# Kernel optimization log

Measured on AMD Instinct MI355X. Metric: run time of the kernel, lower is better.

Reference implementation:

```python
import jax, jax.numpy as jnp
import numpy as np

# static config (matches init_kwargs)
B = 16
S = 32          # patch grid side
td = 2          # tile_dim
ts = td * td    # tile size
T = (S // td) ** 2
R = 1           # register tokens
U = 1           # tile_comp_size
P = S * S
N = R + P
KC = T * U
K = R + KC
D = 768
H = 12
DH = D // H
HID = 32        # CPB hidden


def setup_inputs() -> dict:
    key = jax.random.key(0)
    ks = jax.random.split(key, 11)
    sc = 0.02
    x = jax.random.normal(ks[0], (B, N, D), jnp.float32)
    logit_w = jax.random.normal(ks[1], (U, D), jnp.float32) * sc
    q_w = jax.random.normal(ks[2], (D, D), jnp.float32) * sc
    kv_w = jax.random.normal(ks[3], (2 * D, D), jnp.float32) * sc
    out_w = jax.random.normal(ks[4], (D, D), jnp.float32) * sc
    out_b = jax.random.normal(ks[5], (D,), jnp.float32) * sc
    cpb_w1 = jax.random.normal(ks[6], (HID, 3), jnp.float32) * 0.5
    cpb_b1 = jax.random.normal(ks[7], (HID,), jnp.float32) * sc
    cpb_w2 = jax.random.normal(ks[8], (H, HID), jnp.float32) * 0.1
    cpb_b2 = jax.random.normal(ks[9], (H,), jnp.float32) * sc
    u_pos = jax.random.normal(ks[10], (1, U, 3), jnp.float32) * sc
    # query patch positions [qx, qy, 0] on the SxS grid (row-major)
    coords = np.arange(S, dtype=np.float32)
    gy, gx = np.meshgrid(coords, coords, indexing='ij')
    P_pos = np.stack([gx.ravel(), gy.ravel(), np.zeros(P, np.float32)], axis=-1)[:, None, :]
    # per-tile centers [cx, cy, 0], tile index t = row_tile*(S//td)+col_tile
    tc = np.arange(S // td, dtype=np.float32) * td + (td - 1) / 2.0
    ty, tx = np.meshgrid(tc, tc, indexing='ij')
    tile_centers = np.stack([tx.ravel(), ty.ravel(), np.zeros(T, np.float32)], axis=-1)[:, None, :]
    return {
        'x': x, 'logit_w': logit_w, 'q_w': q_w, 'kv_w': kv_w,
        'out_w': out_w, 'out_b': out_b,
        'cpb_w1': cpb_w1, 'cpb_b1': cpb_b1, 'cpb_w2': cpb_w2, 'cpb_b2': cpb_b2,
        'u_pos': u_pos,
        'P_pos': jnp.asarray(P_pos), 'tile_centers': jnp.asarray(tile_centers),
    }


def _cpb_bias(P_pos, tile_centers, u_pos, cpb_w1, cpb_b1, cpb_w2, cpb_b2, dtype):
    # anchors: tile center + tied per-U offset -> [KC, 3]
    k_pos = (tile_centers + u_pos).reshape(KC, 3)
    delta = P_pos - k_pos[None, :, :].reshape(1, KC, 3)  # [P, KC, 3]
    dxy, s_feat = delta[..., :2], delta[..., 2:]
    phi_xy = jnp.sign(dxy) * jnp.log1p(jnp.abs(dxy))
    feats = jnp.concatenate([phi_xy, -s_feat], axis=-1)  # [P, KC, 3]
    h = jax.nn.gelu(feats @ cpb_w1.T + cpb_b1, approximate=False)
    out_ctx = h @ cpb_w2.T + cpb_b2  # [P, KC, H]
    bias = jnp.zeros((N, K, H), dtype).at[R:, R:, :].set(out_ctx.astype(dtype))
    return bias.transpose(2, 0, 1)  # [H, N, K]


def reference(x, logit_w, q_w, kv_w, out_w, out_b,
              cpb_w1, cpb_b1, cpb_w2, cpb_b2, u_pos, P_pos, tile_centers):
    Bx = x.shape[0]
    # --- tiled softmax-weighted compression ---
    patch = x[:, R:, :].reshape(Bx, S // td, td, S // td, td, D)
    tiled = patch.transpose(0, 1, 3, 2, 4, 5).reshape(Bx, T, ts, D)  # [B,T,ts,D]
    scores = jnp.einsum('btsd,ud->btsu', tiled, logit_w)             # [B,T,ts,U]
    w = jax.nn.softmax(scores.astype(jnp.float32).transpose(0, 1, 3, 2), axis=-1)
    w = w.astype(scores.dtype)                                       # [B,T,U,ts]
    ctx_learn = jnp.einsum('btus,btsd->btud', w, tiled).reshape(Bx, T * U, D)
    ctx = jnp.concatenate([x[:, :R, :], ctx_learn], axis=1)          # [B,K,D]
    # --- projections ---
    q = jnp.einsum('bnd,ed->bne', x, q_w).reshape(Bx, N, H, DH).transpose(0, 2, 1, 3)
    kv = jnp.einsum('bkd,ed->bke', ctx, kv_w).reshape(Bx, K, 2, H, DH)
    k = kv[:, :, 0].transpose(0, 2, 1, 3)  # [B,H,K,DH]
    v = kv[:, :, 1].transpose(0, 2, 1, 3)
    # --- CPB additive bias + SDPA ---
    bias = _cpb_bias(P_pos, tile_centers, u_pos, cpb_w1, cpb_b1, cpb_w2, cpb_b2, x.dtype)
    scale = DH ** -0.5
    logits = jnp.einsum('bhnd,bhkd->bhnk', q, k) * scale + bias[None]
    attn = jax.nn.softmax(logits, axis=-1)
    o = jnp.einsum('bhnk,bhkd->bhnd', attn, v).transpose(0, 2, 1, 3).reshape(Bx, N, D)
    return o @ out_w.T + out_b
```

## Files before the change

### kernel.cpp

```cpp
#include <hip/hip_runtime.h>
#include <math.h>

namespace {
constexpr int BB   = 16;
constexpr int SS   = 32;
constexpr int TT   = 256;
constexpr int PP   = 1024;
constexpr int NTOK = 1025;
constexpr int KCC  = 256;
constexpr int KTOK = 257;
constexpr int DD   = 768;
constexpr int HH   = 12;
constexpr int DHH  = 64;
constexpr int BNP  = 1040;
}

typedef _Float16 f16x8 __attribute__((ext_vector_type(8)));
typedef _Float16 f16x2 __attribute__((ext_vector_type(2)));
typedef float f32x4 __attribute__((ext_vector_type(4)));

#define GLOAD_LDS16(gsrc, ldst)                                               \
  __builtin_amdgcn_global_load_lds(                                           \
      (const __attribute__((address_space(1))) unsigned int*)(gsrc),          \
      (__attribute__((address_space(3))) unsigned int*)(ldst), 16, 0, 0)

__global__ __launch_bounds__(256) void cvt_weights_kernel(
    const float* __restrict__ q_w, const float* __restrict__ kv_w,
    const float* __restrict__ out_w,
    _Float16* __restrict__ qwh, _Float16* __restrict__ kvwh,
    _Float16* __restrict__ owh) {
  constexpr int NQ = DD * DD;
  constexpr int NK = 2 * DD * DD;
  const int i = (blockIdx.x * 256 + threadIdx.x) * 8;
  const float* src;
  _Float16* dst;
  int off;
  float scale = 1.0f;
  if (i < NQ) { src = q_w; dst = qwh; off = i; scale = 0.125f; }
  else if (i < NQ + NK) { src = kv_w; dst = kvwh; off = i - NQ; }
  else if (i < NQ + NK + NQ) { src = out_w; dst = owh; off = i - NQ - NK; }
  else return;
  const float4 a = *(const float4*)(src + off);
  const float4 b = *(const float4*)(src + off + 4);
  f16x8 o;
  o[0] = (_Float16)(a.x * scale); o[1] = (_Float16)(a.y * scale);
  o[2] = (_Float16)(a.z * scale); o[3] = (_Float16)(a.w * scale);
  o[4] = (_Float16)(b.x * scale); o[5] = (_Float16)(b.y * scale);
  o[6] = (_Float16)(b.z * scale); o[7] = (_Float16)(b.w * scale);
  *(f16x8*)(dst + off) = o;
}

__global__ __launch_bounds__(256) void ctx_kernel(
    const float* __restrict__ x, const float* __restrict__ logit_w,
    _Float16* __restrict__ ctxh, _Float16* __restrict__ xh) {
  const int blk = blockIdx.x;
  const int b = blk >> 8;
  const int t = blk & 255;
  const int tid = threadIdx.x;
  const int lane = tid & 63;
  const int w = tid >> 6;
  const float* xb = x + (size_t)b * NTOK * DD;
  _Float16* xhb = xh + (size_t)b * NTOK * DD;

  int prow[4];
#pragma unroll
  for (int s = 0; s < 4; ++s)
    prow[s] = 1 + ((t >> 4) * 2 + (s >> 1)) * SS + ((t & 15) * 2 + (s & 1));

  float sv[3][4];
  float part[4] = {0.f, 0.f, 0.f, 0.f};
#pragma unroll
  for (int it = 0; it < 3; ++it) {
    const int d = tid + 256 * it;
    const float lw = logit_w[d];
#pragma unroll
    for (int s = 0; s < 4; ++s) {
      const float xv = xb[(size_t)prow[s] * DD + d];
      sv[it][s] = xv;
      part[s] += xv * lw;
      xhb[(size_t)prow[s] * DD + d] = (_Float16)xv;
    }
  }

#pragma unroll
  for (int dd = 1; dd < 64; dd <<= 1)
#pragma unroll
    for (int s = 0; s < 4; ++s) part[s] += __shfl_xor(part[s], dd, 64);
  __shared__ float wred[4][4];
  if (lane == 0)
#pragma unroll
    for (int s = 0; s < 4; ++s) wred[w][s] = part[s];
  __syncthreads();
  float score[4];
#pragma unroll
  for (int s = 0; s < 4; ++s)
    score[s] = wred[0][s] + wred[1][s] + wred[2][s] + wred[3][s];

  const float mx = fmaxf(fmaxf(score[0], score[1]), fmaxf(score[2], score[3]));
  float e[4], sum = 0.f;
#pragma unroll
  for (int s = 0; s < 4; ++s) { e[s] = expf(score[s] - mx); sum += e[s]; }
  const float inv = 1.f / sum;
#pragma unroll
  for (int s = 0; s < 4; ++s) e[s] *= inv;

  _Float16* crow = ctxh + ((size_t)b * KTOK + 1 + t) * DD;
#pragma unroll
  for (int it = 0; it < 3; ++it) {
    const int d = tid + 256 * it;
    float acc = 0.f;
#pragma unroll
    for (int s = 0; s < 4; ++s) acc += e[s] * sv[it][s];
    crow[d] = (_Float16)acc;
  }
  if (t == 0) {
    _Float16* dst = ctxh + (size_t)b * KTOK * DD;
#pragma unroll
    for (int it = 0; it < 3; ++it) {
      const int d = tid + 256 * it;
      const float xv = xb[d];
      dst[d] = (_Float16)xv;
      xhb[d] = (_Float16)xv;
    }
  }
}

template <int OUTF16>
__global__ __launch_bounds__(256) void gemm_f16_kernel(
    const _Float16* __restrict__ A, const _Float16* __restrict__ W,
    const float* __restrict__ bias, void* __restrict__ Cout,
    int M, int Nout, int gx) {
  constexpr int BK = 64;
  __shared__ _Float16 As[128 * BK];
  __shared__ _Float16 Ws[128 * BK];

  const int tid = threadIdx.x;
  const int lane = tid & 63;
  const int w = tid >> 6;
  const int fr = lane & 15;
  const int g = lane >> 4;
  const int awm = (w >> 1) * 64;
  const int awn = (w & 1) * 64;

  const int nwg = gridDim.x;
  const int q8 = nwg >> 3, r8 = nwg & 7;
  const int xcd = blockIdx.x & 7;
  const int base = (xcd < r8) ? xcd * (q8 + 1) : r8 * (q8 + 1) + (xcd - r8) * q8;
  const int wg = base + (blockIdx.x >> 3);
  const int row0 = (wg / gx) * 128;
  const int col0 = (wg % gx) * 128;

  const int srow = lane >> 3;
  const int schunk = (lane & 7) ^ (srow & 7);

  f32x4 acc[4][4];
#pragma unroll
  for (int i = 0; i < 4; ++i)
#pragma unroll
    for (int j = 0; j < 4; ++j) acc[i][j] = (f32x4){0.f, 0.f, 0.f, 0.f};

  for (int k0 = 0; k0 < 768; k0 += BK) {
    __syncthreads();
#pragma unroll
    for (int c = 0; c < 4; ++c) {
      const int rl = w * 32 + c * 8 + srow;
      int ga = row0 + rl;
      ga = ga < M ? ga : M - 1;
      GLOAD_LDS16(A + (size_t)ga * 768 + k0 + schunk * 8, &As[(w * 32 + c * 8) * BK]);
      GLOAD_LDS16(W + (size_t)(col0 + rl) * 768 + k0 + schunk * 8,
                  &Ws[(w * 32 + c * 8) * BK]);
    }
    __syncthreads();

#pragma unroll
    for (int ks = 0; ks < 2; ++ks) {
      f16x8 af[4], bf[4];
#pragma unroll
      for (int i = 0; i < 4; ++i) {
        const int row = awm + i * 16 + fr;
        af[i] = *(const f16x8*)&As[row * BK + (((ks * 4 + g) ^ (fr & 7)) * 8)];
      }
#pragma unroll
      for (int j = 0; j < 4; ++j) {
        const int row = awn + j * 16 + fr;
        bf[j] = *(const f16x8*)&Ws[row * BK + (((ks * 4 + g) ^ (fr & 7)) * 8)];
      }
#pragma unroll
      for (int i = 0; i < 4; ++i)
#pragma unroll
        for (int j = 0; j < 4; ++j)
          acc[i][j] = __builtin_amdgcn_mfma_f32_16x16x32_f16(af[i], bf[j], acc[i][j], 0, 0, 0);
    }
  }

#pragma unroll
  for (int i = 0; i < 4; ++i) {
    const int rbase = row0 + awm + i * 16 + g * 4;
#pragma unroll
    for (int reg = 0; reg < 4; ++reg) {
      const int gr = rbase + reg;
      if (gr >= M) continue;
      if constexpr (OUTF16) {
        _Float16* crow = (_Float16*)Cout + (size_t)gr * Nout + col0;
#pragma unroll
        for (int j = 0; j < 4; ++j)
          crow[awn + j * 16 + fr] = (_Float16)acc[i][j][reg];
      } else {
        float* crow = (float*)Cout + (size_t)gr * Nout + col0;
#pragma unroll
        for (int j = 0; j < 4; ++j) {
          const int gc = awn + j * 16 + fr;
          crow[gc] = acc[i][j][reg] + bias[col0 + gc];
        }
      }
    }
  }
}

__global__ __launch_bounds__(256) void cpb_kernel(
    const float* __restrict__ P_pos, const float* __restrict__ tile_centers,
    const float* __restrict__ u_pos,
    const float* __restrict__ w1, const float* __restrict__ b1,
    const float* __restrict__ w2, const float* __restrict__ b2,
    float* __restrict__ biasK) {
  const int idx = blockIdx.x * 256 + threadIdx.x;
  const int c = idx >> 10;
  const int p = idx & 1023;

  const float px = P_pos[p * 3 + 0], py = P_pos[p * 3 + 1], pz = P_pos[p * 3 + 2];
  const float kx = tile_centers[c * 3 + 0] + u_pos[0];
  const float ky = tile_centers[c * 3 + 1] + u_pos[1];
  const float kz = tile_centers[c * 3 + 2] + u_pos[2];
  const float dx = px - kx, dy = py - ky, dz = pz - kz;
  const float fx = copysignf(log1pf(fabsf(dx)), dx);
  const float fy = copysignf(log1pf(fabsf(dy)), dy);
  const float fz = -dz;

  float outh[HH];
#pragma unroll
  for (int h = 0; h < HH; ++h) outh[h] = b2[h];
  for (int j = 0; j < 32; ++j) {
    float hj = fx * w1[j * 3 + 0] + fy * w1[j * 3 + 1] + fz * w1[j * 3 + 2] + b1[j];
    hj = 0.5f * hj * (1.f + erff(hj * 0.70710678118654752f));
#pragma unroll
    for (int h = 0; h < HH; ++h) outh[h] += hj * w2[h * 32 + j];
  }
#pragma unroll
  for (int h = 0; h < HH; ++h) {
    float* row = biasK + ((size_t)h * KCC + c) * BNP;
    row[1 + p] = outh[h];
    if (p == 0) row[0] = 0.f;
    if (p < BNP - 1 - PP) row[1 + PP + p] = 0.f;
  }
}

__global__ __launch_bounds__(512) void attn_mfma_kernel(
    const _Float16* __restrict__ qf, const _Float16* __restrict__ kvf,
    const float* __restrict__ biasK, _Float16* __restrict__ of) {
  __shared__ _Float16 Kh[4][64 * 64];
  __shared__ _Float16 Kt[16 * 64];
  __shared__ _Float16 Vt[4][64 * 64];
  __shared__ _Float16 Vtt[64 * 64];
  __shared__ _Float16 Pl[8][16 * 64];

  const int tid = threadIdx.x;
  const int lane = tid & 63;
  const int w = tid >> 6;
  const int fr = lane & 15;
  const int g = lane >> 4;

  const int b = blockIdx.x / HH;
  const int h = blockIdx.x % HH;

  if (tid < 256) {
    const int ksr = tid >> 2;
    const int kc0 = (tid & 3) * 2;
    const int s7 = ksr & 7;
#pragma unroll
    for (int kt = 0; kt < 4; ++kt) {
      const int key = kt * 64 + ksr;
      const _Float16* srcK = kvf + ((size_t)b * KTOK + key) * (2 * DD) + h * DHH;
      *(f16x8*)&Kh[kt][ksr * 64 + ((kc0 ^ s7) * 8)] = *(const f16x8*)(srcK + kc0 * 8);
      *(f16x8*)&Kh[kt][ksr * 64 + (((kc0 + 1) ^ s7) * 8)] = *(const f16x8*)(srcK + kc0 * 8 + 8);
    }
    if (ksr < 16) {
      const int key = min(256 + ksr, KTOK - 1);
      const _Float16* srcK = kvf + ((size_t)b * KTOK + key) * (2 * DD) + h * DHH;
      *(f16x8*)&Kt[ksr * 64 + ((kc0 ^ s7) * 8)] = *(const f16x8*)(srcK + kc0 * 8);
      *(f16x8*)&Kt[ksr * 64 + (((kc0 + 1) ^ s7) * 8)] = *(const f16x8*)(srcK + kc0 * 8 + 8);
    }
  } else {
    const int t2 = tid - 256;
    const int vkp = t2 & 31;
    const int vdh = (t2 >> 5) * 8;
#pragma unroll
    for (int kt = 0; kt < 4; ++kt) {
      const int kv0 = kt * 64 + 2 * vkp;
      const f16x8 va = *(const f16x8*)(kvf + ((size_t)b * KTOK + kv0) * (2 * DD) + DD + h * DHH + vdh);
      const f16x8 vbv = *(const f16x8*)(kvf + ((size_t)b * KTOK + kv0 + 1) * (2 * DD) + DD + h * DHH + vdh);
#pragma unroll
      for (int e = 0; e < 8; ++e) {
        const int d = vdh + e;
        f16x2 pr; pr[0] = va[e]; pr[1] = vbv[e];
        *(f16x2*)&Vt[kt][d * 64 + (((vkp >> 2) ^ (d & 7)) * 8) + 2 * (vkp & 3)] = pr;
      }
    }
    if (vkp < 16) {
      const int kv0 = min(256 + 2 * vkp, KTOK - 1);
      const int kv1 = min(256 + 2 * vkp + 1, KTOK - 1);
      const f16x8 va = *(const f16x8*)(kvf + ((size_t)b * KTOK + kv0) * (2 * DD) + DD + h * DHH + vdh);
      const f16x8 vbv = *(const f16x8*)(kvf + ((size_t)b * KTOK + kv1) * (2 * DD) + DD + h * DHH + vdh);
#pragma unroll
      for (int e = 0; e < 8; ++e) {
        const int d = vdh + e;
        f16x2 pr; pr[0] = va[e]; pr[1] = vbv[e];
        *(f16x2*)&Vtt[d * 64 + (((vkp >> 2) ^ (d & 7)) * 8) + 2 * (vkp & 3)] = pr;
      }
    }
  }
  __syncthreads();

  for (int c = w; c < 65; c += 8) {
    const int qc = c * 16;

    const int qrow = min(qc + fr, NTOK - 1);
    const _Float16* qsrc = qf + ((size_t)b * NTOK + qrow) * DD + h * DHH;
    f16x8 qa[2];
#pragma unroll
    for (int ks = 0; ks < 2; ++ks)
      qa[ks] = *(const f16x8*)(qsrc + ks * 32 + g * 8);

    float mr_[4], lr_[4];
#pragma unroll
    for (int r = 0; r < 4; ++r) { mr_[r] = -3.0e38f; lr_[r] = 0.f; }
    f32x4 outacc[4];
#pragma unroll
    for (int j = 0; j < 4; ++j) outacc[j] = (f32x4){0.f, 0.f, 0.f, 0.f};

    const int nb = min(qc + g * 4, PP);

#pragma unroll
    for (int kt = 0; kt < 4; ++kt) {
      const int k0 = kt * 64;
      f32x4 sf[4];
      __builtin_amdgcn_s_setprio(1);
#pragma unroll
      for (int f = 0; f < 4; ++f) {
        sf[f] = (f32x4){0.f, 0.f, 0.f, 0.f};
#pragma unroll
        for (int ks = 0; ks < 2; ++ks) {
          const f16x8 kf = *(const f16x8*)&Kh[kt][(f * 16 + fr) * 64 + (((ks * 4 + g) ^ (fr & 7)) * 8)];
          sf[f] = __builtin_amdgcn_mfma_f32_16x16x32_f16(qa[ks], kf, sf[f], 0, 0, 0);
        }
      }
      __builtin_amdgcn_s_setprio(0);

      float pm[4][4];
#pragma unroll
      for (int f = 0; f < 4; ++f) {
        const int key = k0 + f * 16 + fr;
        const int cl = min(max(key - 1, 0), KCC - 1);
        const f32x4 b4 = *(const f32x4*)&biasK[((size_t)h * KCC + cl) * BNP + nb];
        const float bm = (key >= 1) ? 1.f : 0.f;
#pragma unroll
        for (int r = 0; r < 4; ++r) pm[f][r] = sf[f][r] + bm * b4[r];
      }

#pragma unroll
      for (int r = 0; r < 4; ++r) {
        float rm = fmaxf(fmaxf(pm[0][r], pm[1][r]), fmaxf(pm[2][r], pm[3][r]));
#pragma unroll
        for (int d = 1; d < 16; d <<= 1) rm = fmaxf(rm, __shfl_xor(rm, d, 64));
        const float mn = fmaxf(mr_[r], rm);
        const float corr = __expf(mr_[r] - mn);
        mr_[r] = mn;
        float rs = 0.f;
#pragma unroll
        for (int f = 0; f < 4; ++f) {
          const float pv = __expf(pm[f][r] - mn);
          pm[f][r] = pv;
          rs += pv;
        }
#pragma unroll
        for (int d = 1; d < 16; d <<= 1) rs += __shfl_xor(rs, d, 64);
        lr_[r] = lr_[r] * corr + rs;
#pragma unroll
        for (int j = 0; j < 4; ++j) outacc[j][r] *= corr;
      }

#pragma unroll
      for (int f = 0; f < 4; ++f)
#pragma unroll
        for (int r = 0; r < 4; ++r) {
          const int prw = g * 4 + r;
          Pl[w][prw * 64 + (((2 * f + (fr >> 3)) ^ (prw & 7)) * 8) + (fr & 7)] =
              (_Float16)pm[f][r];
        }

      __builtin_amdgcn_s_setprio(1);
#pragma unroll
      for (int ks = 0; ks < 2; ++ks) {
        const f16x8 pa = *(const f16x8*)&Pl[w][fr * 64 + (((ks * 4 + g) ^ (fr & 7)) * 8)];
#pragma unroll
        for (int j = 0; j < 4; ++j) {
          const f16x8 vbf = *(const f16x8*)&Vt[kt][(j * 16 + fr) * 64 + (((ks * 4 + g) ^ (fr & 7)) * 8)];
          outacc[j] = __builtin_amdgcn_mfma_f32_16x16x32_f16(pa, vbf, outacc[j], 0, 0, 0);
        }
      }
      __builtin_amdgcn_s_setprio(0);
    }

    {
      f32x4 sf0 = (f32x4){0.f, 0.f, 0.f, 0.f};
#pragma unroll
      for (int ks = 0; ks < 2; ++ks) {
        const f16x8 kf = *(const f16x8*)&Kt[fr * 64 + (((ks * 4 + g) ^ (fr & 7)) * 8)];
        sf0 = __builtin_amdgcn_mfma_f32_16x16x32_f16(qa[ks], kf, sf0, 0, 0, 0);
      }
      const f32x4 b4 = *(const f32x4*)&biasK[((size_t)h * KCC + (KCC - 1)) * BNP + nb];
      float pm0[4];
#pragma unroll
      for (int r = 0; r < 4; ++r)
        pm0[r] = (fr == 0) ? (sf0[r] + b4[r]) : -3.0e38f;

#pragma unroll
      for (int r = 0; r < 4; ++r) {
        float rm = pm0[r];
#pragma unroll
        for (int d = 1; d < 16; d <<= 1) rm = fmaxf(rm, __shfl_xor(rm, d, 64));
        const float mn = fmaxf(mr_[r], rm);
        const float corr = __expf(mr_[r] - mn);
        mr_[r] = mn;
        float pv = __expf(pm0[r] - mn);
        pm0[r] = pv;
        float rs = pv;
#pragma unroll
        for (int d = 1; d < 16; d <<= 1) rs += __shfl_xor(rs, d, 64);
        lr_[r] = lr_[r] * corr + rs;
#pragma unroll
        for (int j = 0; j < 4; ++j) outacc[j][r] *= corr;
      }

#pragma unroll
      for (int r = 0; r < 4; ++r) {
        const int prw = g * 4 + r;
        Pl[w][prw * 64 + (((fr >> 3) ^ (prw & 7)) * 8) + (fr & 7)] = (_Float16)pm0[r];
        Pl[w][prw * 64 + (((2 + (fr >> 3)) ^ (prw & 7)) * 8) + (fr & 7)] = (_Float16)0.f;
      }

      const f16x8 pa = *(const f16x8*)&Pl[w][fr * 64 + ((g ^ (fr & 7)) * 8)];
#pragma unroll
      for (int j = 0; j < 4; ++j) {
        const f16x8 vbf = *(const f16x8*)&Vtt[(j * 16 + fr) * 64 + ((g ^ (fr & 7)) * 8)];
        outacc[j] = __builtin_amdgcn_mfma_f32_16x16x32_f16(pa, vbf, outacc[j], 0, 0, 0);
      }
    }

#pragma unroll
    for (int r = 0; r < 4; ++r) {
      const int n = qc + g * 4 + r;
      if (n >= NTOK) continue;
      const float inv = 1.f / lr_[r];
      _Float16* orow = of + ((size_t)b * NTOK + n) * DD + h * DHH + fr;
#pragma unroll
      for (int j = 0; j < 4; ++j) orow[j * 16] = (_Float16)(outacc[j][r] * inv);
    }
  }
}

extern "C" void kernel_launch(void* const* d_in, const int* in_sizes, int n_in,
                              void* d_out, int out_size, void* d_ws, size_t ws_size,
                              hipStream_t stream) {
  const float* x            = (const float*)d_in[0];
  const float* logit_w      = (const float*)d_in[1];
  const float* q_w          = (const float*)d_in[2];
  const float* kv_w         = (const float*)d_in[3];
  const float* out_w        = (const float*)d_in[4];
  const float* out_b        = (const float*)d_in[5];
  const float* cpb_w1       = (const float*)d_in[6];
  const float* cpb_b1       = (const float*)d_in[7];
  const float* cpb_w2       = (const float*)d_in[8];
  const float* cpb_b2       = (const float*)d_in[9];
  const float* u_pos        = (const float*)d_in[10];
  const float* P_pos        = (const float*)d_in[11];
  const float* tile_centers = (const float*)d_in[12];
  float* out = (float*)d_out;

  const int Mq  = BB * NTOK;
  const int Mkv = BB * KTOK;

  char* p = (char*)d_ws;
  auto alloc = [&](size_t bytes) {
    char* r = p;
    p += (bytes + 255) & ~(size_t)255;
    return r;
  };
  _Float16* xh    = (_Float16*)alloc((size_t)Mq * DD * 2);
  _Float16* ctxh  = (_Float16*)alloc((size_t)Mkv * DD * 2);
  _Float16* qwh   = (_Float16*)alloc((size_t)DD * DD * 2);
  _Float16* kvwh  = (_Float16*)alloc((size_t)2 * DD * DD * 2);
  _Float16* owh   = (_Float16*)alloc((size_t)DD * DD * 2);
  _Float16* qbuf  = (_Float16*)alloc((size_t)Mq * DD * 2);
  _Float16* kvbuf = (_Float16*)alloc((size_t)Mkv * 2 * DD * 2);
  float*    biasK = (float*)alloc((size_t)HH * KCC * BNP * 4);
  _Float16* obuf  = (_Float16*)alloc((size_t)Mq * DD * 2);

  const int n_wt = 4 * DD * DD;

  cvt_weights_kernel<<<(n_wt / 8 + 255) / 256, 256, 0, stream>>>(
      q_w, kv_w, out_w, qwh, kvwh, owh);

  ctx_kernel<<<BB * TT, 256, 0, stream>>>(x, logit_w, ctxh, xh);

  const int gq = 6 * 129;
  const int gk = 12 * 33;
  gemm_f16_kernel<1><<<gq, 256, 0, stream>>>(xh, qwh, nullptr, qbuf, Mq, DD, 6);
  gemm_f16_kernel<1><<<gk, 256, 0, stream>>>(ctxh, kvwh, nullptr, kvbuf, Mkv, 2 * DD, 12);

  cpb_kernel<<<(PP * KCC) / 256, 256, 0, stream>>>(
      P_pos, tile_centers, u_pos, cpb_w1, cpb_b1, cpb_w2, cpb_b2, biasK);

  attn_mfma_kernel<<<BB * HH, 512, 0, stream>>>(qbuf, kvbuf, biasK, obuf);

  gemm_f16_kernel<0><<<gq, 256, 0, stream>>>(obuf, owh, out_b, out, Mq, DD, 6);
}
```

Before: 198.9 us.

## Split attention query chunks across two blocks and handle tail key in registers

Launches twice as many attention blocks, each handling half the query chunks of a (batch, head) pair, with an XCD-aware block-to-group mapping. The single leftover key (index 256) is now handled with a scalar dot product and register FMA instead of a padded 16-key MFMA tile through LDS. This removes the Kt/Vtt shared arrays and their padded loads. The cost is that each block reloads the full K/V tiles for its half, doubling K/V staging traffic.

```diff
diff --git a/kernel.cpp b/kernel.cpp
--- a/kernel.cpp
+++ b/kernel.cpp
@@ -258,9 +258,7 @@
     const _Float16* __restrict__ qf, const _Float16* __restrict__ kvf,
     const float* __restrict__ biasK, _Float16* __restrict__ of) {
   __shared__ _Float16 Kh[4][64 * 64];
-  __shared__ _Float16 Kt[16 * 64];
   __shared__ _Float16 Vt[4][64 * 64];
-  __shared__ _Float16 Vtt[64 * 64];
   __shared__ _Float16 Pl[8][16 * 64];
 
   const int tid = threadIdx.x;
@@ -269,8 +267,12 @@
   const int fr = lane & 15;
   const int g = lane >> 4;
 
-  const int b = blockIdx.x / HH;
-  const int h = blockIdx.x % HH;
+  const int xcd = blockIdx.x & 7;
+  const int s = blockIdx.x >> 3;
+  const int grp = xcd + 8 * (s >> 1);
+  const int half = s & 1;
+  const int b = grp / HH;
+  const int h = grp % HH;
 
   if (tid < 256) {
     const int ksr = tid >> 2;
@@ -283,12 +285,6 @@
       *(f16x8*)&Kh[kt][ksr * 64 + ((kc0 ^ s7) * 8)] = *(const f16x8*)(srcK + kc0 * 8);
       *(f16x8*)&Kh[kt][ksr * 64 + (((kc0 + 1) ^ s7) * 8)] = *(const f16x8*)(srcK + kc0 * 8 + 8);
     }
-    if (ksr < 16) {
-      const int key = min(256 + ksr, KTOK - 1);
-      const _Float16* srcK = kvf + ((size_t)b * KTOK + key) * (2 * DD) + h * DHH;
-      *(f16x8*)&Kt[ksr * 64 + ((kc0 ^ s7) * 8)] = *(const f16x8*)(srcK + kc0 * 8);
-      *(f16x8*)&Kt[ksr * 64 + (((kc0 + 1) ^ s7) * 8)] = *(const f16x8*)(srcK + kc0 * 8 + 8);
-    }
   } else {
     const int t2 = tid - 256;
     const int vkp = t2 & 31;
@@ -305,22 +301,22 @@
         *(f16x2*)&Vt[kt][d * 64 + (((vkp >> 2) ^ (d & 7)) * 8) + 2 * (vkp & 3)] = pr;
       }
     }
-    if (vkp < 16) {
-      const int kv0 = min(256 + 2 * vkp, KTOK - 1);
-      const int kv1 = min(256 + 2 * vkp + 1, KTOK - 1);
-      const f16x8 va = *(const f16x8*)(kvf + ((size_t)b * KTOK + kv0) * (2 * DD) + DD + h * DHH + vdh);
-      const f16x8 vbv = *(const f16x8*)(kvf + ((size_t)b * KTOK + kv1) * (2 * DD) + DD + h * DHH + vdh);
-#pragma unroll
-      for (int e = 0; e < 8; ++e) {
-        const int d = vdh + e;
-        f16x2 pr; pr[0] = va[e]; pr[1] = vbv[e];
-        *(f16x2*)&Vtt[d * 64 + (((vkp >> 2) ^ (d & 7)) * 8) + 2 * (vkp & 3)] = pr;
-      }
-    }
-  }
+  }
+
+  const _Float16* k256p = kvf + ((size_t)b * KTOK + 256) * (2 * DD) + h * DHH;
+  f16x8 kt256[2];
+#pragma unroll
+  for (int ks = 0; ks < 2; ++ks)
+    kt256[ks] = *(const f16x8*)(k256p + ks * 32 + g * 8);
+  float v256[4];
+#pragma unroll
+  for (int j = 0; j < 4; ++j) v256[j] = (float)k256p[DD + j * 16 + fr];
+
   __syncthreads();
 
-  for (int c = w; c < 65; c += 8) {
+  const int cstart = half ? 33 : 0;
+  const int cend = half ? 65 : 33;
+  for (int c = cstart + w; c < cend; c += 8) {
     const int qc = c * 16;
 
     const int qrow = min(qc + fr, NTOK - 1);
@@ -411,48 +407,26 @@
     }
 
     {
-      f32x4 sf0 = (f32x4){0.f, 0.f, 0.f, 0.f};
-#pragma unroll
-      for (int ks = 0; ks < 2; ++ks) {
-        const f16x8 kf = *(const f16x8*)&Kt[fr * 64 + (((ks * 4 + g) ^ (fr & 7)) * 8)];
-        sf0 = __builtin_amdgcn_mfma_f32_16x16x32_f16(qa[ks], kf, sf0, 0, 0, 0);
-      }
-      const f32x4 b4 = *(const f32x4*)&biasK[((size_t)h * KCC + (KCC - 1)) * BNP + nb];
-      float pm0[4];
-#pragma unroll
-      for (int r = 0; r < 4; ++r)
-        pm0[r] = (fr == 0) ? (sf0[r] + b4[r]) : -3.0e38f;
-
+      float sp = 0.f;
+#pragma unroll
+      for (int ks = 0; ks < 2; ++ks)
+#pragma unroll
+        for (int j = 0; j < 8; ++j)
+          sp += (float)qa[ks][j] * (float)kt256[ks][j];
+      sp += __shfl_xor(sp, 16, 64);
+      sp += __shfl_xor(sp, 32, 64);
+      const f32x4 bt = *(const f32x4*)&biasK[((size_t)h * KCC + (KCC - 1)) * BNP + nb];
 #pragma unroll
       for (int r = 0; r < 4; ++r) {
-        float rm = pm0[r];
-#pragma unroll
-        for (int d = 1; d < 16; d <<= 1) rm = fmaxf(rm, __shfl_xor(rm, d, 64));
-        const float mn = fmaxf(mr_[r], rm);
+        const float s256 = __shfl(sp, g * 4 + r, 64) + bt[r];
+        const float mn = fmaxf(mr_[r], s256);
         const float corr = __expf(mr_[r] - mn);
+        const float pv = __expf(s256 - mn);
         mr_[r] = mn;
-        float pv = __expf(pm0[r] - mn);
-        pm0[r] = pv;
-        float rs = pv;
-#pragma unroll
-        for (int d = 1; d < 16; d <<= 1) rs += __shfl_xor(rs, d, 64);
-        lr_[r] = lr_[r] * corr + rs;
-#pragma unroll
-        for (int j = 0; j < 4; ++j) outacc[j][r] *= corr;
-      }
-
-#pragma unroll
-      for (int r = 0; r < 4; ++r) {
-        const int prw = g * 4 + r;
-        Pl[w][prw * 64 + (((fr >> 3) ^ (prw & 7)) * 8) + (fr & 7)] = (_Float16)pm0[r];
-        Pl[w][prw * 64 + (((2 + (fr >> 3)) ^ (prw & 7)) * 8) + (fr & 7)] = (_Float16)0.f;
-      }
-
-      const f16x8 pa = *(const f16x8*)&Pl[w][fr * 64 + ((g ^ (fr & 7)) * 8)];
-#pragma unroll
-      for (int j = 0; j < 4; ++j) {
-        const f16x8 vbf = *(const f16x8*)&Vtt[(j * 16 + fr) * 64 + ((g ^ (fr & 7)) * 8)];
-        outacc[j] = __builtin_amdgcn_mfma_f32_16x16x32_f16(pa, vbf, outacc[j], 0, 0, 0);
+        lr_[r] = lr_[r] * corr + pv;
+#pragma unroll
+        for (int j = 0; j < 4; ++j)
+          outacc[j][r] = outacc[j][r] * corr + pv * v256[j];
       }
     }
 
@@ -520,7 +494,7 @@
   cpb_kernel<<<(PP * KCC) / 256, 256, 0, stream>>>(
       P_pos, tile_centers, u_pos, cpb_w1, cpb_b1, cpb_w2, cpb_b2, biasK);
 
-  attn_mfma_kernel<<<BB * HH, 512, 0, stream>>>(qbuf, kvbuf, biasK, obuf);
+  attn_mfma_kernel<<<2 * BB * HH, 512, 0, stream>>>(qbuf, kvbuf, biasK, obuf);
 
   gemm_f16_kernel<0><<<gq, 256, 0, stream>>>(obuf, owh, out_b, out, Mq, DD, 6);
 }
```

Result: slower. 206.1 us (+3.6%).
